# Kernel optimization log

Hardware: AMD Instinct MI355X
Metric: run time of the kernel (lower is better)

## Reference

```python
import jax, jax.numpy as jnp
import numpy as np

B, N = 2048, 2048

def setup_inputs() -> dict:
    key = jax.random.key(0)
    k1, k2, k3 = jax.random.split(key, 3)
    src_coords = jax.random.normal(k1, (B, N, 3), dtype=jnp.float32)
    tgt_coords = jax.random.normal(k2, (B, N, 3), dtype=jnp.float32)
    weights = jax.random.uniform(k3, (B, 1, N), dtype=jnp.float32)
    return {"src_coords": src_coords, "tgt_coords": tgt_coords, "weights": weights}

def reference(src_coords, tgt_coords, weights):
    # (b,N,3) -> (b,3,N), matching torch transpose(2,1)
    src = jnp.swapaxes(src_coords, 1, 2)
    tgt = jnp.swapaxes(tgt_coords, 1, 2)
    # total weight per batch (b,1,1)
    w = jnp.sum(weights, axis=2, keepdims=True) + 1e-4
    # weighted centroids (b,3,1)
    src_centroid = jnp.sum(src * weights, axis=2, keepdims=True) / w
    tgt_centroid = jnp.sum(tgt * weights, axis=2, keepdims=True) / w
    src_centered = src - src_centroid
    tgt_centered = tgt - tgt_centroid
    # weighted cross-covariance (b,3,3): bmm(tgt_centered*weights, src_centered^T)/w
    W = jnp.einsum('bin,bjn->bij', tgt_centered * weights, src_centered) / w
    U, _, Vh = jnp.linalg.svd(W)  # torch.svd returns V; Vh = V^T, det(V)=det(Vh)
    det_UV = jnp.linalg.det(U) * jnp.linalg.det(Vh)
    # S = diag(1, 1, det_UV)
    s = jnp.stack([jnp.ones_like(det_UV), jnp.ones_like(det_UV), det_UV], axis=-1)
    # R = U @ diag(s) @ V^T
    R_tgt_src = jnp.einsum('bij,bj,bjk->bik', U, s, Vh)
    # t_tgt_src_insrc = src_centroid - R^T @ tgt_centroid
    t_tgt_src_insrc = src_centroid - jnp.einsum('bji,bjk->bik', R_tgt_src, tgt_centroid)
    t_src_tgt_intgt = -jnp.einsum('bij,bjk->bik', R_tgt_src, t_tgt_src_insrc)
    return (R_tgt_src, t_src_tgt_intgt)
```

## Files before the change

### kernel.cpp

```cpp
#include <hip/hip_runtime.h>
#include <math.h>

#define B_BATCH 2048
#define N_PTS   2048

__global__ __launch_bounds__(256) void reduce_kernel(
    const float* __restrict__ src, const float* __restrict__ tgt,
    const float* __restrict__ wts, float* __restrict__ sums)
{
    const int b   = blockIdx.x;
    const int tid = threadIdx.x;
    const float* sb = src + (size_t)b * N_PTS * 3;
    const float* tb = tgt + (size_t)b * N_PTS * 3;
    const float* wb = wts + (size_t)b * N_PTS;

    float acc[16];
#pragma unroll
    for (int i = 0; i < 16; ++i) acc[i] = 0.f;

#pragma unroll
    for (int it = 0; it < N_PTS / 256; ++it) {
        const int n = tid + it * 256;
        const float w  = wb[n];
        const float sx = sb[3*n+0], sy = sb[3*n+1], sz = sb[3*n+2];
        const float tx = tb[3*n+0], ty = tb[3*n+1], tz = tb[3*n+2];
        const float wsx = w * sx, wsy = w * sy, wsz = w * sz;
        acc[0]  += w;
        acc[1]  += wsx;      acc[2]  += wsy;      acc[3]  += wsz;
        acc[4]  += w * tx;   acc[5]  += w * ty;   acc[6]  += w * tz;
        acc[7]  += tx * wsx; acc[8]  += tx * wsy; acc[9]  += tx * wsz;
        acc[10] += ty * wsx; acc[11] += ty * wsy; acc[12] += ty * wsz;
        acc[13] += tz * wsx; acc[14] += tz * wsy; acc[15] += tz * wsz;
    }

#pragma unroll
    for (int i = 0; i < 16; ++i) {
#pragma unroll
        for (int off = 32; off > 0; off >>= 1)
            acc[i] += __shfl_down(acc[i], off, 64);
    }

    __shared__ float red[4][16];
    const int lane = tid & 63, wv = tid >> 6;
    if (lane == 0) {
#pragma unroll
        for (int i = 0; i < 16; ++i) red[wv][i] = acc[i];
    }
    __syncthreads();
    if (tid < 16)
        sums[(size_t)b * 16 + tid] =
            red[0][tid] + red[1][tid] + red[2][tid] + red[3][tid];
}

__global__ __launch_bounds__(256) void svd_kernel(
    const float* __restrict__ sums,
    float* __restrict__ outR, float* __restrict__ outT)
{
    const int b = blockIdx.x * blockDim.x + threadIdx.x;
    if (b >= B_BATCH) return;
    const float* S = sums + (size_t)b * 16;

    const double wtot = (double)S[0] + 1e-4;
    const double inv  = 1.0 / wtot;
    double sc[3] = { S[1]*inv, S[2]*inv, S[3]*inv };
    double tc[3] = { S[4]*inv, S[5]*inv, S[6]*inv };
    const double f = (wtot + 1e-4) * inv;

    double W[3][3];
#pragma unroll
    for (int i = 0; i < 3; ++i)
#pragma unroll
        for (int j = 0; j < 3; ++j)
            W[i][j] = (double)S[7 + 3*i + j] * inv - f * tc[i] * sc[j];

    double A[3][3];
    for (int i = 0; i < 3; ++i)
        for (int j = 0; j < 3; ++j) {
            double s = 0.0;
            for (int k = 0; k < 3; ++k) s += W[k][i] * W[k][j];
            A[i][j] = s;
        }

    double V[3][3] = {{1,0,0},{0,1,0},{0,0,1}};
    for (int sweep = 0; sweep < 15; ++sweep) {
        double offd = fabs(A[0][1]) + fabs(A[0][2]) + fabs(A[1][2]);
        if (offd < 1e-300) break;
        for (int pq = 0; pq < 3; ++pq) {
            const int p = (pq == 2) ? 1 : 0;
            const int q = (pq == 0) ? 1 : 2;
            const double apq = A[p][q];
            if (fabs(apq) == 0.0) continue;
            const double tau = (A[q][q] - A[p][p]) / (2.0 * apq);
            const double tt  = (tau >= 0.0 ? 1.0 : -1.0) /
                               (fabs(tau) + sqrt(1.0 + tau * tau));
            const double c = 1.0 / sqrt(1.0 + tt * tt);
            const double s = tt * c;
            for (int k = 0; k < 3; ++k) {
                const double akp = A[k][p], akq = A[k][q];
                A[k][p] = c * akp - s * akq;
                A[k][q] = s * akp + c * akq;
            }
            for (int k = 0; k < 3; ++k) {
                const double apk = A[p][k], aqk = A[q][k];
                A[p][k] = c * apk - s * aqk;
                A[q][k] = s * apk + c * aqk;
            }
            for (int k = 0; k < 3; ++k) {
                const double vkp = V[k][p], vkq = V[k][q];
                V[k][p] = c * vkp - s * vkq;
                V[k][q] = s * vkp + c * vkq;
            }
        }
    }

    double lam[3] = { A[0][0], A[1][1], A[2][2] };
    int idx[3] = {0, 1, 2};
    if (lam[idx[0]] < lam[idx[1]]) { int t_ = idx[0]; idx[0] = idx[1]; idx[1] = t_; }
    if (lam[idx[0]] < lam[idx[2]]) { int t_ = idx[0]; idx[0] = idx[2]; idx[2] = t_; }
    if (lam[idx[1]] < lam[idx[2]]) { int t_ = idx[1]; idx[1] = idx[2]; idx[2] = t_; }

    double v[3][3];
#pragma unroll
    for (int c = 0; c < 3; ++c)
        for (int r = 0; r < 3; ++r) v[r][c] = V[r][idx[c]];

    double u[3][3];
    double col[3];
    for (int r = 0; r < 3; ++r)
        col[r] = W[r][0]*v[0][0] + W[r][1]*v[1][0] + W[r][2]*v[2][0];
    double s0 = sqrt(col[0]*col[0] + col[1]*col[1] + col[2]*col[2]);
    if (s0 > 1e-150) {
        for (int r = 0; r < 3; ++r) u[r][0] = col[r] / s0;
    } else {
        u[0][0] = 1.0; u[1][0] = 0.0; u[2][0] = 0.0;
    }
    for (int r = 0; r < 3; ++r)
        col[r] = W[r][0]*v[0][1] + W[r][1]*v[1][1] + W[r][2]*v[2][1];
    {
        double d01 = col[0]*u[0][0] + col[1]*u[1][0] + col[2]*u[2][0];
        for (int r = 0; r < 3; ++r) col[r] -= d01 * u[r][0];
        double s1 = sqrt(col[0]*col[0] + col[1]*col[1] + col[2]*col[2]);
        if (s1 > 1e-12 * (1.0 + s0)) {
            for (int r = 0; r < 3; ++r) u[r][1] = col[r] / s1;
        } else {
            double ax = fabs(u[0][0]), ay = fabs(u[1][0]), az = fabs(u[2][0]);
            double e[3] = {0, 0, 0};
            if (ax <= ay && ax <= az) e[0] = 1.0;
            else if (ay <= az)        e[1] = 1.0;
            else                      e[2] = 1.0;
            double p0 = u[1][0]*e[2] - u[2][0]*e[1];
            double p1 = u[2][0]*e[0] - u[0][0]*e[2];
            double p2 = u[0][0]*e[1] - u[1][0]*e[0];
            double pn = sqrt(p0*p0 + p1*p1 + p2*p2);
            u[0][1] = p0/pn; u[1][1] = p1/pn; u[2][1] = p2/pn;
        }
    }
    for (int r = 0; r < 3; ++r)
        col[r] = W[r][0]*v[0][2] + W[r][1]*v[1][2] + W[r][2]*v[2][2];
    {
        double d02 = col[0]*u[0][0] + col[1]*u[1][0] + col[2]*u[2][0];
        double d12 = col[0]*u[0][1] + col[1]*u[1][1] + col[2]*u[2][1];
        for (int r = 0; r < 3; ++r) col[r] -= d02 * u[r][0] + d12 * u[r][1];
        double s2 = sqrt(col[0]*col[0] + col[1]*col[1] + col[2]*col[2]);
        if (s2 > 1e-12 * (1.0 + s0)) {
            for (int r = 0; r < 3; ++r) u[r][2] = col[r] / s2;
        } else {
            u[0][2] = u[1][0]*u[2][1] - u[2][0]*u[1][1];
            u[1][2] = u[2][0]*u[0][1] - u[0][0]*u[2][1];
            u[2][2] = u[0][0]*u[1][1] - u[1][0]*u[0][1];
        }
    }

    double detU =
        u[0][0]*(u[1][1]*u[2][2] - u[2][1]*u[1][2]) -
        u[0][1]*(u[1][0]*u[2][2] - u[2][0]*u[1][2]) +
        u[0][2]*(u[1][0]*u[2][1] - u[2][0]*u[1][1]);
    double detV =
        v[0][0]*(v[1][1]*v[2][2] - v[2][1]*v[1][2]) -
        v[0][1]*(v[1][0]*v[2][2] - v[2][0]*v[1][2]) +
        v[0][2]*(v[1][0]*v[2][1] - v[2][0]*v[1][1]);
    const double d = (detU * detV >= 0.0) ? 1.0 : -1.0;

    double R[3][3];
#pragma unroll
    for (int r = 0; r < 3; ++r)
#pragma unroll
        for (int c = 0; c < 3; ++c)
            R[r][c] = u[r][0]*v[c][0] + u[r][1]*v[c][1] + d * u[r][2]*v[c][2];

    float* Rb = outR + (size_t)b * 9;
#pragma unroll
    for (int r = 0; r < 3; ++r)
#pragma unroll
        for (int c = 0; c < 3; ++c)
            Rb[3*r + c] = (float)R[r][c];

    float* Tb = outT + (size_t)b * 3;
#pragma unroll
    for (int r = 0; r < 3; ++r)
        Tb[r] = (float)(tc[r] - (R[r][0]*sc[0] + R[r][1]*sc[1] + R[r][2]*sc[2]));
}

extern "C" void kernel_launch(void* const* d_in, const int* in_sizes, int n_in,
                              void* d_out, int out_size, void* d_ws, size_t ws_size,
                              hipStream_t stream) {
    const float* src = (const float*)d_in[0];
    const float* tgt = (const float*)d_in[1];
    const float* wts = (const float*)d_in[2];
    float* outR = (float*)d_out;
    float* outT = outR + (size_t)B_BATCH * 9;
    float* sums = (float*)d_ws;

    reduce_kernel<<<B_BATCH, 256, 0, stream>>>(src, tgt, wts, sums);
    svd_kernel<<<(B_BATCH + 255) / 256, 256, 0, stream>>>(sums, outR, outT);
}
```

Before: 153.3 us.

## Stage point data through LDS with float4 loads and tighten Jacobi convergence

The reduction kernel now loads src, tgt and weights in 512-point chunks as coalesced float4 loads into shared memory, and each thread then reads its stride-3 xyz triples from LDS. This replaces the strided per-thread scalar global loads. The SVD kernel caps Jacobi sweeps at 8 and stops on a relative off-diagonal tolerance, which trims iterations in the small per-batch kernel. Costs are two barriers per chunk, about 16KB of LDS per block, and possibly slightly different convergence behaviour.

```diff
diff --git a/kernel.cpp b/kernel.cpp
--- a/kernel.cpp
+++ b/kernel.cpp
@@ -3,6 +3,10 @@
 
 #define B_BATCH 2048
 #define N_PTS   2048
+#define CHUNK   512
+#define NCHUNK  (N_PTS / CHUNK)
+#define CF4     (CHUNK * 3 / 4)
+#define WF4     (CHUNK / 4)
 
 __global__ __launch_bounds__(256) void reduce_kernel(
     const float* __restrict__ src, const float* __restrict__ tgt,
@@ -10,27 +14,48 @@
 {
     const int b   = blockIdx.x;
     const int tid = threadIdx.x;
-    const float* sb = src + (size_t)b * N_PTS * 3;
-    const float* tb = tgt + (size_t)b * N_PTS * 3;
-    const float* wb = wts + (size_t)b * N_PTS;
+
+    const float4* s4 = (const float4*)(src + (size_t)b * N_PTS * 3);
+    const float4* t4 = (const float4*)(tgt + (size_t)b * N_PTS * 3);
+    const float4* w4 = (const float4*)(wts + (size_t)b * N_PTS);
+
+    __shared__ float s_s[CHUNK * 3];
+    __shared__ float s_t[CHUNK * 3];
+    __shared__ float s_w[CHUNK];
 
     float acc[16];
 #pragma unroll
     for (int i = 0; i < 16; ++i) acc[i] = 0.f;
 
-#pragma unroll
-    for (int it = 0; it < N_PTS / 256; ++it) {
-        const int n = tid + it * 256;
-        const float w  = wb[n];
-        const float sx = sb[3*n+0], sy = sb[3*n+1], sz = sb[3*n+2];
-        const float tx = tb[3*n+0], ty = tb[3*n+1], tz = tb[3*n+2];
-        const float wsx = w * sx, wsy = w * sy, wsz = w * sz;
-        acc[0]  += w;
-        acc[1]  += wsx;      acc[2]  += wsy;      acc[3]  += wsz;
-        acc[4]  += w * tx;   acc[5]  += w * ty;   acc[6]  += w * tz;
-        acc[7]  += tx * wsx; acc[8]  += tx * wsy; acc[9]  += tx * wsz;
-        acc[10] += ty * wsx; acc[11] += ty * wsy; acc[12] += ty * wsz;
-        acc[13] += tz * wsx; acc[14] += tz * wsy; acc[15] += tz * wsz;
+    for (int c = 0; c < NCHUNK; ++c) {
+        float4* ds = (float4*)s_s;
+        float4* dt = (float4*)s_t;
+        float4* dw = (float4*)s_w;
+        const int cbase = c * CF4;
+        ds[tid] = s4[cbase + tid];
+        dt[tid] = t4[cbase + tid];
+        if (tid < CF4 - 256) {
+            ds[256 + tid] = s4[cbase + 256 + tid];
+            dt[256 + tid] = t4[cbase + 256 + tid];
+        }
+        if (tid < WF4) dw[tid] = w4[c * WF4 + tid];
+        __syncthreads();
+
+#pragma unroll
+        for (int k = 0; k < CHUNK / 256; ++k) {
+            const int p = tid + k * 256;
+            const float w  = s_w[p];
+            const float sx = s_s[3*p+0], sy = s_s[3*p+1], sz = s_s[3*p+2];
+            const float tx = s_t[3*p+0], ty = s_t[3*p+1], tz = s_t[3*p+2];
+            const float wsx = w * sx, wsy = w * sy, wsz = w * sz;
+            acc[0]  += w;
+            acc[1]  += wsx;      acc[2]  += wsy;      acc[3]  += wsz;
+            acc[4]  += w * tx;   acc[5]  += w * ty;   acc[6]  += w * tz;
+            acc[7]  += tx * wsx; acc[8]  += tx * wsy; acc[9]  += tx * wsz;
+            acc[10] += ty * wsx; acc[11] += ty * wsy; acc[12] += ty * wsz;
+            acc[13] += tz * wsx; acc[14] += tz * wsy; acc[15] += tz * wsz;
+        }
+        __syncthreads();
     }
 
 #pragma unroll
@@ -82,9 +107,10 @@
         }
 
     double V[3][3] = {{1,0,0},{0,1,0},{0,0,1}};
-    for (int sweep = 0; sweep < 15; ++sweep) {
+    const double tr0 = fabs(A[0][0]) + fabs(A[1][1]) + fabs(A[2][2]) + 1e-300;
+    for (int sweep = 0; sweep < 8; ++sweep) {
         double offd = fabs(A[0][1]) + fabs(A[0][2]) + fabs(A[1][2]);
-        if (offd < 1e-300) break;
+        if (offd <= 1e-28 * tr0) break;
         for (int pq = 0; pq < 3; ++pq) {
             const int p = (pq == 2) ? 1 : 0;
             const int q = (pq == 0) ? 1 : 2;
```

Result: no change. 154.7 us (+0.9%).

## Vectorize reduce loads as contiguous float4 chunks, relax Jacobi convergence, shrink SVD blocks

Applied to the files above, without the earlier changes.

Each thread in the reduction now loads 8 contiguous points as float4 vectors (6 for src, 6 for tgt, 2 for weights) instead of strided scalar loads, so each access is a wide contiguous read. The SVD kernel switches to 64-thread blocks to spread 2048 batch items over 32 blocks instead of 8. Its Jacobi sweep now stops early on a relative off-diagonal tolerance and is capped at 8 sweeps. The relative tolerance could change accuracy slightly in degenerate cases, and the per-thread contiguous layout makes lanes access memory with a stride of 96 bytes rather than fully coalesced consecutive addresses.

```diff
diff --git a/kernel.cpp b/kernel.cpp
--- a/kernel.cpp
+++ b/kernel.cpp
@@ -10,20 +10,32 @@
 {
     const int b   = blockIdx.x;
     const int tid = threadIdx.x;
-    const float* sb = src + (size_t)b * N_PTS * 3;
-    const float* tb = tgt + (size_t)b * N_PTS * 3;
-    const float* wb = wts + (size_t)b * N_PTS;
+
+    const float4* s4 = (const float4*)(src + (size_t)b * N_PTS * 3);
+    const float4* t4 = (const float4*)(tgt + (size_t)b * N_PTS * 3);
+    const float4* w4 = (const float4*)(wts + (size_t)b * N_PTS);
+
+    float4 sv[6], tv[6], wv[2];
+#pragma unroll
+    for (int k = 0; k < 6; ++k) sv[k] = s4[6 * tid + k];
+#pragma unroll
+    for (int k = 0; k < 6; ++k) tv[k] = t4[6 * tid + k];
+    wv[0] = w4[2 * tid];
+    wv[1] = w4[2 * tid + 1];
+
+    const float* sf = (const float*)sv;
+    const float* tf = (const float*)tv;
+    const float* wf = (const float*)wv;
 
     float acc[16];
 #pragma unroll
     for (int i = 0; i < 16; ++i) acc[i] = 0.f;
 
 #pragma unroll
-    for (int it = 0; it < N_PTS / 256; ++it) {
-        const int n = tid + it * 256;
-        const float w  = wb[n];
-        const float sx = sb[3*n+0], sy = sb[3*n+1], sz = sb[3*n+2];
-        const float tx = tb[3*n+0], ty = tb[3*n+1], tz = tb[3*n+2];
+    for (int p = 0; p < 8; ++p) {
+        const float w  = wf[p];
+        const float sx = sf[3*p+0], sy = sf[3*p+1], sz = sf[3*p+2];
+        const float tx = tf[3*p+0], ty = tf[3*p+1], tz = tf[3*p+2];
         const float wsx = w * sx, wsy = w * sy, wsz = w * sz;
         acc[0]  += w;
         acc[1]  += wsx;      acc[2]  += wsy;      acc[3]  += wsz;
@@ -41,10 +53,10 @@
     }
 
     __shared__ float red[4][16];
-    const int lane = tid & 63, wv = tid >> 6;
+    const int lane = tid & 63, wv_ = tid >> 6;
     if (lane == 0) {
 #pragma unroll
-        for (int i = 0; i < 16; ++i) red[wv][i] = acc[i];
+        for (int i = 0; i < 16; ++i) red[wv_][i] = acc[i];
     }
     __syncthreads();
     if (tid < 16)
@@ -52,7 +64,7 @@
             red[0][tid] + red[1][tid] + red[2][tid] + red[3][tid];
 }
 
-__global__ __launch_bounds__(256) void svd_kernel(
+__global__ __launch_bounds__(64) void svd_kernel(
     const float* __restrict__ sums,
     float* __restrict__ outR, float* __restrict__ outT)
 {
@@ -82,9 +94,10 @@
         }
 
     double V[3][3] = {{1,0,0},{0,1,0},{0,0,1}};
-    for (int sweep = 0; sweep < 15; ++sweep) {
+    const double tr0 = fabs(A[0][0]) + fabs(A[1][1]) + fabs(A[2][2]) + 1e-300;
+    for (int sweep = 0; sweep < 8; ++sweep) {
         double offd = fabs(A[0][1]) + fabs(A[0][2]) + fabs(A[1][2]);
-        if (offd < 1e-300) break;
+        if (offd <= 1e-28 * tr0) break;
         for (int pq = 0; pq < 3; ++pq) {
             const int p = (pq == 2) ? 1 : 0;
             const int q = (pq == 0) ? 1 : 2;
@@ -212,5 +225,5 @@
     float* sums = (float*)d_ws;
 
     reduce_kernel<<<B_BATCH, 256, 0, stream>>>(src, tgt, wts, sums);
-    svd_kernel<<<(B_BATCH + 255) / 256, 256, 0, stream>>>(sums, outR, outT);
+    svd_kernel<<<B_BATCH / 64, 64, 0, stream>>>(sums, outR, outT);
 }
```

Result: faster. 148.7 us (-3.0%).
